# Optimization experiments

Hardware: AMD Instinct MI355X
Metric: run time of the kernel (lower is better)

## Reference

```python
import jax, jax.numpy as jnp
import numpy as np

N_HEAD = 8
LN_EPS = 1e-6


def setup_inputs() -> dict:
    key = jax.random.key(0)
    ks = jax.random.split(key, 6)
    B, S, D = 4, 2048, 256  # D = hidden_size*2 = input_dim
    sc = 1.0 / np.sqrt(D)
    return {
        "inputs": jax.random.normal(ks[0], (B, S, D), jnp.float32),
        "Wq": jax.random.normal(ks[1], (D, D), jnp.float32) * sc,
        "Wk": jax.random.normal(ks[2], (D, D), jnp.float32) * sc,
        "Wv": jax.random.normal(ks[3], (D, D), jnp.float32) * sc,
        "Wf": jax.random.normal(ks[4], (D, D), jnp.float32) * sc,
        "bf": jnp.zeros((D,), jnp.float32),
        "gamma": jnp.ones((D,), jnp.float32),
        "beta": jnp.zeros((D,), jnp.float32),
    }


def reference(inputs, Wq, Wk, Wv, Wf, bf, gamma, beta):
    B, S, D = inputs.shape
    H = N_HEAD
    dh = D // H
    # Projections (torch Linear: x @ W.T), no bias for Q/K/V
    Q = (inputs @ Wq.T).reshape(B, S, H, dh)
    K = (inputs @ Wk.T).reshape(B, S, H, dh)
    V = (inputs @ Wv.T).reshape(B, S, H, dh)
    # NOTE: original scales by sqrt(K.shape[1]) == sqrt(seq_len), not sqrt(dh)
    scale = 1.0 / jnp.sqrt(jnp.float32(S)).astype(inputs.dtype)
    scores = jnp.einsum("bqhd,bkhd->bhqk", Q, K) * scale  # [B,H,S,S]
    attn = jax.nn.softmax(scores, axis=-1)
    out = jnp.einsum("bhqk,bkhd->bqhd", attn, V).reshape(B, S, D)
    out = out @ Wf.T + bf
    # residual + LayerNorm(eps=1e-6)
    x = inputs + out
    mu = jnp.mean(x, axis=-1, keepdims=True)
    var = jnp.mean(jnp.square(x - mu), axis=-1, keepdims=True)
    return (x - mu) * jax.lax.rsqrt(var + LN_EPS) * gamma + beta
```

## Files before the change

kernel.cpp:

```cpp
#include <hip/hip_runtime.h>
#include <hip/hip_bf16.h>

typedef __attribute__((ext_vector_type(8))) short short8;
typedef __attribute__((ext_vector_type(4))) float f32x4;
typedef __attribute__((ext_vector_type(16))) float f32x16;

#define DEVI __device__ __forceinline__

DEVI unsigned short f2bf(float f) {
  union { float f; unsigned int u; } v; v.f = f;
  unsigned int r = v.u + 0x7fffu + ((v.u >> 16) & 1u);
  return (unsigned short)(r >> 16);
}

DEVI unsigned int cvt2(float lo, float hi) {
  unsigned int r;
  asm("v_cvt_pk_bf16_f32 %0, %1, %2" : "=v"(r) : "v"(lo), "v"(hi));
  return r;
}

#define GLDS16(gp, lp)                                                         \
  __builtin_amdgcn_global_load_lds(                                            \
      (const __attribute__((address_space(1))) unsigned int*)(uintptr_t)(gp),  \
      (__attribute__((address_space(3))) unsigned int*)(uintptr_t)(lp), 16, 0, 0)

#define SB 4
#define SS 2048
#define SD 256
#define SH 8
#define SDH 32
#define SM 8192

#define QSCALE 0.0318793654f

#define Q_OFF   0
#define K_OFF   (SM * SD)
#define VT_OFF  (2 * SM * SD)
#define AO_OFF  (3 * SM * SD)

__global__ __launch_bounds__(256) void qkv_k(
    const float* __restrict__ X, const float* __restrict__ Wq,
    const float* __restrict__ Wk, const float* __restrict__ Wv,
    unsigned short* __restrict__ ws) {
  __shared__ __align__(16) unsigned short Atile[128][72];
  __shared__ __align__(16) unsigned short Btile[128][72];
  int tid = threadIdx.x, w = tid >> 6, lane = tid & 63, g = lane >> 4, r = lane & 15;
  int m0 = blockIdx.x * 128, n0 = blockIdx.y * 128;
  int z = n0 >> 8, nbase = n0 & 255;
  const float* Wz = (z == 0) ? Wq : (z == 1) ? Wk : Wv;
  int wr = (w >> 1) * 64, wc = (w & 1) * 64;
  f32x4 acc[4][4] = {};
  int srow = tid >> 3, scol = (tid & 7) * 8;
  float4 a0[4], a1[4], b0[4], b1[4];
#pragma unroll
  for (int p = 0; p < 4; ++p) {
    const float* xa = X + (m0 + srow + p * 32) * SD + scol;
    const float* xb = Wz + (nbase + srow + p * 32) * SD + scol;
    a0[p] = *reinterpret_cast<const float4*>(xa);
    a1[p] = *reinterpret_cast<const float4*>(xa + 4);
    b0[p] = *reinterpret_cast<const float4*>(xb);
    b1[p] = *reinterpret_cast<const float4*>(xb + 4);
  }
  for (int k0 = 0; k0 < SD; k0 += 64) {
    __syncthreads();
#pragma unroll
    for (int p = 0; p < 4; ++p) {
      uint4 ua = { cvt2(a0[p].x, a0[p].y), cvt2(a0[p].z, a0[p].w),
                   cvt2(a1[p].x, a1[p].y), cvt2(a1[p].z, a1[p].w) };
      uint4 ub = { cvt2(b0[p].x, b0[p].y), cvt2(b0[p].z, b0[p].w),
                   cvt2(b1[p].x, b1[p].y), cvt2(b1[p].z, b1[p].w) };
      *reinterpret_cast<uint4*>(&Atile[srow + p * 32][scol]) = ua;
      *reinterpret_cast<uint4*>(&Btile[srow + p * 32][scol]) = ub;
    }
    __syncthreads();
    if (k0 + 64 < SD) {
#pragma unroll
      for (int p = 0; p < 4; ++p) {
        const float* xa = X + (m0 + srow + p * 32) * SD + k0 + 64 + scol;
        const float* xb = Wz + (nbase + srow + p * 32) * SD + k0 + 64 + scol;
        a0[p] = *reinterpret_cast<const float4*>(xa);
        a1[p] = *reinterpret_cast<const float4*>(xa + 4);
        b0[p] = *reinterpret_cast<const float4*>(xb);
        b1[p] = *reinterpret_cast<const float4*>(xb + 4);
      }
    }
#pragma unroll
    for (int ks = 0; ks < 2; ++ks) {
      short8 af[4], bf[4];
#pragma unroll
      for (int i = 0; i < 4; ++i)
        af[i] = *reinterpret_cast<const short8*>(&Atile[wr + i * 16 + r][ks * 32 + g * 8]);
#pragma unroll
      for (int j = 0; j < 4; ++j)
        bf[j] = *reinterpret_cast<const short8*>(&Btile[wc + j * 16 + r][ks * 32 + g * 8]);
#pragma unroll
      for (int i = 0; i < 4; ++i)
#pragma unroll
        for (int j = 0; j < 4; ++j)
          acc[i][j] = __builtin_amdgcn_mfma_f32_16x16x32_bf16(af[i], bf[j], acc[i][j], 0, 0, 0);
    }
  }
  int b_ = m0 >> 11, sbase = m0 & 2047;
  float qs = (z == 0) ? QSCALE : 1.0f;
  unsigned short* Vt = &Btile[0][0];
#pragma unroll
  for (int p = 0; p < 2; ++p) {
    __syncthreads();
    if ((w & 1) == p) {
      if (z < 2) {
#pragma unroll
        for (int i = 0; i < 4; ++i)
#pragma unroll
          for (int j = 0; j < 4; ++j)
#pragma unroll
            for (int jj = 0; jj < 4; ++jj)
              Atile[wr + i * 16 + g * 4 + jj][j * 16 + r] = f2bf(acc[i][j][jj] * qs);
      } else {
#pragma unroll
        for (int i = 0; i < 4; ++i)
#pragma unroll
          for (int j = 0; j < 4; ++j) {
            unsigned short o4[4];
#pragma unroll
            for (int jj = 0; jj < 4; ++jj) o4[jj] = f2bf(acc[i][j][jj]);
            *reinterpret_cast<uint2*>(&Vt[(j * 16 + r) * 136 + wr + i * 16 + g * 4]) =
                *reinterpret_cast<const uint2*>(o4);
          }
      }
    }
    __syncthreads();
    if (z < 2) {
      unsigned short* out = ws + (z == 0 ? Q_OFF : K_OFF);
      int h0 = (nbase + p * 64) >> 5;
#pragma unroll
      for (int it = 0; it < 4; ++it) {
        int c = it * 256 + tid;
        int m = c >> 3, cr = c & 7, hl = cr >> 2, ch = cr & 3;
        short8 val = *reinterpret_cast<const short8*>(&Atile[m][hl * 32 + ch * 8]);
        int h = h0 + hl;
        *reinterpret_cast<short8*>(
            out + (((b_ << 3) + h) * SS + sbase + m) * SDH + ch * 8) = val;
      }
    } else {
      unsigned short* out = ws + VT_OFF;
      int nb = nbase + p * 64;
#pragma unroll
      for (int it = 0; it < 4; ++it) {
        int c = it * 256 + tid;
        int nl = c >> 4, ch = c & 15;
        short8 val = *reinterpret_cast<const short8*>(&Vt[nl * 136 + ch * 8]);
        int col = nb + nl, h = col >> 5, d = col & 31;
        *reinterpret_cast<short8*>(
            out + ((((b_ << 3) + h) << 5) + d) * SS + sbase + ch * 8) = val;
      }
    }
  }
}

__global__ __launch_bounds__(512, 4) void attn_k(const unsigned short* __restrict__ ws_c,
                                                 unsigned short* __restrict__ ws) {
  __shared__ __align__(16) unsigned char smem[65536];
  int tid = threadIdx.x, w = tid >> 6, lane = tid & 63;
  int wg = w >> 2, wl = w & 3, gtid = tid & 255;
  int n32 = lane & 31, hi = lane >> 5;
  int wgid = ((blockIdx.x & 7) << 6) + (blockIdx.x >> 3);
  int bh = wgid >> 4, qb = wgid & 15;
  int q0 = qb * 128 + wl * 32;
  const unsigned short* Qh = ws_c + Q_OFF + bh * (SS * SDH);
  const unsigned short* Kg = ws_c + K_OFF + (bh * SS + wg * 1024) * SDH;
  const unsigned short* Vg = ws_c + VT_OFF + bh * (SDH * SS) + wg * 1024;
  short8 qB0 = *reinterpret_cast<const short8*>(Qh + (q0 + n32) * SDH + 8 * hi);
  short8 qB1 = *reinterpret_cast<const short8*>(Qh + (q0 + n32) * SDH + 16 + 8 * hi);
  unsigned short* Kbuf0 = (unsigned short*)(smem + wg * 16384);
  unsigned short* Kbuf1 = (unsigned short*)(smem + wg * 16384 + 8192);
  unsigned short* Vbuf0 = (unsigned short*)(smem + 32768 + wg * 16384);
  unsigned short* Vbuf1 = (unsigned short*)(smem + 32768 + wg * 16384 + 8192);
  int wv = gtid >> 6;
  int kr = gtid >> 2;
  int kcg = (gtid & 3) ^ ((kr >> 1) & 3);
  const unsigned short* gK0 = Kg + kr * SDH + kcg * 8;
  const unsigned short* gK1 = gK0 + 64 * SDH;
  int vr = gtid >> 4;
  int vcg = (gtid & 15) ^ (vr & 7);
  const unsigned short* gV0 = Vg + vr * SS + vcg * 8;
  const unsigned short* gV1 = gV0 + 16 * SS;
  auto issue = [&](int buf, int tt) {
    char* kd = (char*)(buf ? Kbuf1 : Kbuf0) + wv * 1024;
    char* vd = (char*)(buf ? Vbuf1 : Vbuf0) + wv * 1024;
    GLDS16(gK0 + tt * 4096, kd);
    GLDS16(gK1 + tt * 4096, kd + 4096);
    GLDS16(gV0 + tt * 128, vd);
    GLDS16(gV1 + tt * 128, vd + 4096);
  };
  issue(0, 0);
  f32x16 O = {}, Lf = {};
  union { unsigned int u[4]; short8 sv; } ONES;
  ONES.u[0] = 0x3F803F80u; ONES.u[1] = 0x3F803F80u;
  ONES.u[2] = 0x3F803F80u; ONES.u[3] = 0x3F803F80u;
  int rb = (n32 >> 1) & 3;
  int koff0 = (hi ^ rb) * 8;
  int koff1 = ((2 + hi) ^ rb) * 8;
  int vb7 = n32 & 7;
  for (int t = 0; t < 8; ++t) {
    const unsigned short* Kt = (t & 1) ? Kbuf1 : Kbuf0;
    const unsigned short* Vt = (t & 1) ? Vbuf1 : Vbuf0;
    if (t < 7) {
      issue((t + 1) & 1, t + 1);
      asm volatile("s_waitcnt vmcnt(4)" ::: "memory");
    } else {
      asm volatile("s_waitcnt vmcnt(0)" ::: "memory");
    }
    __builtin_amdgcn_s_barrier();
#pragma unroll
    for (int si = 0; si < 4; ++si) {
      int s = (si + wl) & 3;
      const unsigned short* krow = Kt + (s * 32 + n32) * 32;
      short8 ka = *reinterpret_cast<const short8*>(krow + koff0);
      short8 kb = *reinterpret_cast<const short8*>(krow + koff1);
      f32x16 aC = {};
      __builtin_amdgcn_s_setprio(1);
      aC = __builtin_amdgcn_mfma_f32_32x32x16_bf16(ka, qB0, aC, 0, 0, 0);
      aC = __builtin_amdgcn_mfma_f32_32x32x16_bf16(kb, qB1, aC, 0, 0, 0);
      __builtin_amdgcn_s_setprio(0);
#pragma unroll
      for (int i = 0; i < 16; ++i) aC[i] = __builtin_amdgcn_exp2f(aC[i]);
      unsigned int pk[8];
#pragma unroll
      for (int i = 0; i < 8; ++i) pk[i] = cvt2(aC[2 * i], aC[2 * i + 1]);
      asm("v_permlane32_swap_b32 %0, %1" : "+v"(pk[0]), "+v"(pk[2]));
      asm("v_permlane32_swap_b32 %0, %1" : "+v"(pk[1]), "+v"(pk[3]));
      asm("v_permlane32_swap_b32 %0, %1" : "+v"(pk[4]), "+v"(pk[6]));
      asm("v_permlane32_swap_b32 %0, %1" : "+v"(pk[5]), "+v"(pk[7]));
      union { unsigned int u[4]; short8 sv; } A1, A2;
      A1.u[0] = pk[0]; A1.u[1] = pk[1]; A1.u[2] = pk[2]; A1.u[3] = pk[3];
      A2.u[0] = pk[4]; A2.u[1] = pk[5]; A2.u[2] = pk[6]; A2.u[3] = pk[7];
      const unsigned short* vrow = Vt + n32 * 128;
      short8 vB0 = *reinterpret_cast<const short8*>(vrow + ((s * 4 + hi) ^ vb7) * 8);
      short8 vB1 = *reinterpret_cast<const short8*>(vrow + ((s * 4 + 2 + hi) ^ vb7) * 8);
      __builtin_amdgcn_s_setprio(1);
      O  = __builtin_amdgcn_mfma_f32_32x32x16_bf16(A1.sv, vB0, O, 0, 0, 0);
      O  = __builtin_amdgcn_mfma_f32_32x32x16_bf16(A2.sv, vB1, O, 0, 0, 0);
      Lf = __builtin_amdgcn_mfma_f32_32x32x16_bf16(A1.sv, ONES.sv, Lf, 0, 0, 0);
      Lf = __builtin_amdgcn_mfma_f32_32x32x16_bf16(A2.sv, ONES.sv, Lf, 0, 0, 0);
      __builtin_amdgcn_s_setprio(0);
    }
    __builtin_amdgcn_s_barrier();
  }
  __syncthreads();
  float* OCf = reinterpret_cast<float*>(smem);
  float* LCf = OCf + 16 * 257;
  int p = wl * 64 + lane;
  if (wg == 1) {
#pragma unroll
    for (int i = 0; i < 16; ++i) { OCf[i * 257 + p] = O[i]; LCf[i * 257 + p] = Lf[i]; }
  }
  __syncthreads();
  if (wg == 0) {
    int b = bh >> 3, h = bh & 7;
    unsigned short* AO = ws + AO_OFF;
#pragma unroll
    for (int rr = 0; rr < 16; ++rr) {
      float Ot = O[rr] + OCf[rr * 257 + p];
      float Lt = Lf[rr] + LCf[rr * 257 + p];
      int q = (rr & 3) + 8 * (rr >> 2) + 4 * hi;
      AO[(b * SS + q0 + q) * SD + h * SDH + n32] = f2bf(Ot / Lt);
    }
  }
}

__global__ __launch_bounds__(256) void final_k(
    const unsigned short* __restrict__ ws_c, const float* __restrict__ X,
    const float* __restrict__ Wf, const float* __restrict__ bfv,
    const float* __restrict__ gamma, const float* __restrict__ beta,
    float* __restrict__ out) {
  __shared__ __align__(16) unsigned short Al[32][72];
  __shared__ __align__(16) unsigned short Bl[256][72];
  __shared__ float Cl[32][257];
  const unsigned short* AO = ws_c + AO_OFF;
  int tid = threadIdx.x, w = tid >> 6, lane = tid & 63, g = lane >> 4, r = lane & 15;
  int m0 = blockIdx.x * 32;
  f32x4 acc[2][4] = {};
  int arow = tid >> 3, acol = (tid & 7) * 8;
  for (int k0 = 0; k0 < SD; k0 += 64) {
    short8 av = *reinterpret_cast<const short8*>(AO + (m0 + arow) * SD + k0 + acol);
    float4 w0[8], w1[8];
#pragma unroll
    for (int i = 0; i < 8; i++) {
      const float* wp = Wf + (i * 32 + arow) * SD + k0 + acol;
      w0[i] = *reinterpret_cast<const float4*>(wp);
      w1[i] = *reinterpret_cast<const float4*>(wp + 4);
    }
    __syncthreads();
    *reinterpret_cast<short8*>(&Al[arow][acol]) = av;
#pragma unroll
    for (int i = 0; i < 8; i++) {
      uint4 ub = { cvt2(w0[i].x, w0[i].y), cvt2(w0[i].z, w0[i].w),
                   cvt2(w1[i].x, w1[i].y), cvt2(w1[i].z, w1[i].w) };
      *reinterpret_cast<uint4*>(&Bl[i * 32 + arow][acol]) = ub;
    }
    __syncthreads();
#pragma unroll
    for (int ks = 0; ks < 2; ks++) {
      short8 af0 = *reinterpret_cast<const short8*>(&Al[r][ks * 32 + g * 8]);
      short8 af1 = *reinterpret_cast<const short8*>(&Al[16 + r][ks * 32 + g * 8]);
#pragma unroll
      for (int nt = 0; nt < 4; nt++) {
        short8 bb = *reinterpret_cast<const short8*>(&Bl[w * 64 + nt * 16 + r][ks * 32 + g * 8]);
        acc[0][nt] = __builtin_amdgcn_mfma_f32_16x16x32_bf16(af0, bb, acc[0][nt], 0, 0, 0);
        acc[1][nt] = __builtin_amdgcn_mfma_f32_16x16x32_bf16(af1, bb, acc[1][nt], 0, 0, 0);
      }
    }
  }
#pragma unroll
  for (int rt = 0; rt < 2; rt++)
#pragma unroll
    for (int nt = 0; nt < 4; nt++)
#pragma unroll
      for (int j = 0; j < 4; j++)
        Cl[rt * 16 + g * 4 + j][w * 64 + nt * 16 + r] = acc[rt][nt][j];
  __syncthreads();
  int row = tid >> 3, sub = tid & 7;
  int m = m0 + row;
  float x[32];
  float sum = 0.f, sumsq = 0.f;
#pragma unroll
  for (int i = 0; i < 8; i++) {
    int col = sub * 32 + i * 4;
    float4 xv = *reinterpret_cast<const float4*>(X + m * SD + col);
    float4 bb = *reinterpret_cast<const float4*>(bfv + col);
    x[i * 4 + 0] = Cl[row][col + 0] + xv.x + bb.x;
    x[i * 4 + 1] = Cl[row][col + 1] + xv.y + bb.y;
    x[i * 4 + 2] = Cl[row][col + 2] + xv.z + bb.z;
    x[i * 4 + 3] = Cl[row][col + 3] + xv.w + bb.w;
  }
#pragma unroll
  for (int c = 0; c < 32; c++) { sum += x[c]; sumsq += x[c] * x[c]; }
  sum += __shfl_xor(sum, 1);  sumsq += __shfl_xor(sumsq, 1);
  sum += __shfl_xor(sum, 2);  sumsq += __shfl_xor(sumsq, 2);
  sum += __shfl_xor(sum, 4);  sumsq += __shfl_xor(sumsq, 4);
  float mean = sum * (1.0f / 256.0f);
  float var = sumsq * (1.0f / 256.0f) - mean * mean;
  float rstd = rsqrtf(var + 1e-6f);
#pragma unroll
  for (int i = 0; i < 8; i++) {
    int col = sub * 32 + i * 4;
    float4 gv = *reinterpret_cast<const float4*>(gamma + col);
    float4 bv2 = *reinterpret_cast<const float4*>(beta + col);
    float4 ov;
    ov.x = (x[i * 4 + 0] - mean) * rstd * gv.x + bv2.x;
    ov.y = (x[i * 4 + 1] - mean) * rstd * gv.y + bv2.y;
    ov.z = (x[i * 4 + 2] - mean) * rstd * gv.z + bv2.z;
    ov.w = (x[i * 4 + 3] - mean) * rstd * gv.w + bv2.w;
    *reinterpret_cast<float4*>(out + m * SD + col) = ov;
  }
}

extern "C" void kernel_launch(void* const* d_in, const int* in_sizes, int n_in,
                              void* d_out, int out_size, void* d_ws, size_t ws_size,
                              hipStream_t stream) {
  const float* X  = (const float*)d_in[0];
  const float* Wq = (const float*)d_in[1];
  const float* Wk = (const float*)d_in[2];
  const float* Wv = (const float*)d_in[3];
  const float* Wf = (const float*)d_in[4];
  const float* bf = (const float*)d_in[5];
  const float* gm = (const float*)d_in[6];
  const float* bt = (const float*)d_in[7];
  float* out = (float*)d_out;
  unsigned short* ws = (unsigned short*)d_ws;

  qkv_k<<<dim3(64, 6), 256, 0, stream>>>(X, Wq, Wk, Wv, ws);
  attn_k<<<dim3(512), 512, 0, stream>>>(ws, ws);
  final_k<<<256, 256, 0, stream>>>(ws, X, Wf, bf, gm, bt, out);
}
```

Before: 58.94 us.

## Halve GEMM row tiles and pre-convert Wf to bf16 in projection kernel

The QKV projection kernel now uses 64-row tiles, doubling its grid to 768 blocks, and the output kernel uses 16-row tiles over 512 blocks. This puts more workgroups on the GPU's compute units. Wf is converted to bf16 once inside the projection kernel by the V-projection blocks and stored in workspace, so the final kernel loads bf16 weights directly instead of reloading and converting fp32 Wf in every block. In exchange, each block reuses loaded weight tiles less, and the workspace grows by one extra weight region.

```diff
diff --git a/kernel.cpp b/kernel.cpp
--- a/kernel.cpp
+++ b/kernel.cpp
@@ -37,64 +37,78 @@
 #define K_OFF   (SM * SD)
 #define VT_OFF  (2 * SM * SD)
 #define AO_OFF  (3 * SM * SD)
+#define WF_OFF  (4 * SM * SD)
 
 __global__ __launch_bounds__(256) void qkv_k(
     const float* __restrict__ X, const float* __restrict__ Wq,
     const float* __restrict__ Wk, const float* __restrict__ Wv,
-    unsigned short* __restrict__ ws) {
-  __shared__ __align__(16) unsigned short Atile[128][72];
+    const float* __restrict__ Wf, unsigned short* __restrict__ ws) {
+  __shared__ __align__(16) unsigned short Atile[64][72];
   __shared__ __align__(16) unsigned short Btile[128][72];
   int tid = threadIdx.x, w = tid >> 6, lane = tid & 63, g = lane >> 4, r = lane & 15;
-  int m0 = blockIdx.x * 128, n0 = blockIdx.y * 128;
-  int z = n0 >> 8, nbase = n0 & 255;
+  int m0 = blockIdx.x * 64;
+  int z = blockIdx.y >> 1, nbase = (blockIdx.y & 1) * 128;
   const float* Wz = (z == 0) ? Wq : (z == 1) ? Wk : Wv;
-  int wr = (w >> 1) * 64, wc = (w & 1) * 64;
-  f32x4 acc[4][4] = {};
+  if (z == 2) {
+    int slice = blockIdx.x + (nbase ? 128 : 0);
+    ws[WF_OFF + slice * 256 + tid] = f2bf(Wf[slice * 256 + tid]);
+  }
+  int wr = (w >> 1) * 32, wc = (w & 1) * 64;
+  f32x4 acc[2][4] = {};
   int srow = tid >> 3, scol = (tid & 7) * 8;
-  float4 a0[4], a1[4], b0[4], b1[4];
-#pragma unroll
-  for (int p = 0; p < 4; ++p) {
+  float4 a0[2], a1[2], b0[4], b1[4];
+#pragma unroll
+  for (int p = 0; p < 2; ++p) {
     const float* xa = X + (m0 + srow + p * 32) * SD + scol;
-    const float* xb = Wz + (nbase + srow + p * 32) * SD + scol;
     a0[p] = *reinterpret_cast<const float4*>(xa);
     a1[p] = *reinterpret_cast<const float4*>(xa + 4);
+  }
+#pragma unroll
+  for (int p = 0; p < 4; ++p) {
+    const float* xb = Wz + (nbase + srow + p * 32) * SD + scol;
     b0[p] = *reinterpret_cast<const float4*>(xb);
     b1[p] = *reinterpret_cast<const float4*>(xb + 4);
   }
   for (int k0 = 0; k0 < SD; k0 += 64) {
     __syncthreads();
 #pragma unroll
-    for (int p = 0; p < 4; ++p) {
+    for (int p = 0; p < 2; ++p) {
       uint4 ua = { cvt2(a0[p].x, a0[p].y), cvt2(a0[p].z, a0[p].w),
                    cvt2(a1[p].x, a1[p].y), cvt2(a1[p].z, a1[p].w) };
+      *reinterpret_cast<uint4*>(&Atile[srow + p * 32][scol]) = ua;
+    }
+#pragma unroll
+    for (int p = 0; p < 4; ++p) {
       uint4 ub = { cvt2(b0[p].x, b0[p].y), cvt2(b0[p].z, b0[p].w),
                    cvt2(b1[p].x, b1[p].y), cvt2(b1[p].z, b1[p].w) };
-      *reinterpret_cast<uint4*>(&Atile[srow + p * 32][scol]) = ua;
       *reinterpret_cast<uint4*>(&Btile[srow + p * 32][scol]) = ub;
     }
     __syncthreads();
     if (k0 + 64 < SD) {
 #pragma unroll
-      for (int p = 0; p < 4; ++p) {
+      for (int p = 0; p < 2; ++p) {
         const float* xa = X + (m0 + srow + p * 32) * SD + k0 + 64 + scol;
-        const float* xb = Wz + (nbase + srow + p * 32) * SD + k0 + 64 + scol;
         a0[p] = *reinterpret_cast<const float4*>(xa);
         a1[p] = *reinterpret_cast<const float4*>(xa + 4);
+      }
+#pragma unroll
+      for (int p = 0; p < 4; ++p) {
+        const float* xb = Wz + (nbase + srow + p * 32) * SD + k0 + 64 + scol;
         b0[p] = *reinterpret_cast<const float4*>(xb);
         b1[p] = *reinterpret_cast<const float4*>(xb + 4);
       }
     }
 #pragma unroll
     for (int ks = 0; ks < 2; ++ks) {
-      short8 af[4], bf[4];
-#pragma unroll
-      for (int i = 0; i < 4; ++i)
+      short8 af[2], bf[4];
+#pragma unroll
+      for (int i = 0; i < 2; ++i)
         af[i] = *reinterpret_cast<const short8*>(&Atile[wr + i * 16 + r][ks * 32 + g * 8]);
 #pragma unroll
       for (int j = 0; j < 4; ++j)
         bf[j] = *reinterpret_cast<const short8*>(&Btile[wc + j * 16 + r][ks * 32 + g * 8]);
 #pragma unroll
-      for (int i = 0; i < 4; ++i)
+      for (int i = 0; i < 2; ++i)
 #pragma unroll
         for (int j = 0; j < 4; ++j)
           acc[i][j] = __builtin_amdgcn_mfma_f32_16x16x32_bf16(af[i], bf[j], acc[i][j], 0, 0, 0);
@@ -109,7 +123,7 @@
     if ((w & 1) == p) {
       if (z < 2) {
 #pragma unroll
-        for (int i = 0; i < 4; ++i)
+        for (int i = 0; i < 2; ++i)
 #pragma unroll
           for (int j = 0; j < 4; ++j)
 #pragma unroll
@@ -117,13 +131,13 @@
               Atile[wr + i * 16 + g * 4 + jj][j * 16 + r] = f2bf(acc[i][j][jj] * qs);
       } else {
 #pragma unroll
-        for (int i = 0; i < 4; ++i)
+        for (int i = 0; i < 2; ++i)
 #pragma unroll
           for (int j = 0; j < 4; ++j) {
             unsigned short o4[4];
 #pragma unroll
             for (int jj = 0; jj < 4; ++jj) o4[jj] = f2bf(acc[i][j][jj]);
-            *reinterpret_cast<uint2*>(&Vt[(j * 16 + r) * 136 + wr + i * 16 + g * 4]) =
+            *reinterpret_cast<uint2*>(&Vt[(j * 16 + r) * 80 + wr + i * 16 + g * 4]) =
                 *reinterpret_cast<const uint2*>(o4);
           }
       }
@@ -133,7 +147,7 @@
       unsigned short* out = ws + (z == 0 ? Q_OFF : K_OFF);
       int h0 = (nbase + p * 64) >> 5;
 #pragma unroll
-      for (int it = 0; it < 4; ++it) {
+      for (int it = 0; it < 2; ++it) {
         int c = it * 256 + tid;
         int m = c >> 3, cr = c & 7, hl = cr >> 2, ch = cr & 3;
         short8 val = *reinterpret_cast<const short8*>(&Atile[m][hl * 32 + ch * 8]);
@@ -145,10 +159,10 @@
       unsigned short* out = ws + VT_OFF;
       int nb = nbase + p * 64;
 #pragma unroll
-      for (int it = 0; it < 4; ++it) {
+      for (int it = 0; it < 2; ++it) {
         int c = it * 256 + tid;
-        int nl = c >> 4, ch = c & 15;
-        short8 val = *reinterpret_cast<const short8*>(&Vt[nl * 136 + ch * 8]);
+        int nl = c >> 3, ch = c & 7;
+        short8 val = *reinterpret_cast<const short8*>(&Vt[nl * 80 + ch * 8]);
         int col = nb + nl, h = col >> 5, d = col & 31;
         *reinterpret_cast<short8*>(
             out + ((((b_ << 3) + h) << 5) + d) * SS + sbase + ch * 8) = val;
@@ -270,62 +284,53 @@
 
 __global__ __launch_bounds__(256) void final_k(
     const unsigned short* __restrict__ ws_c, const float* __restrict__ X,
-    const float* __restrict__ Wf, const float* __restrict__ bfv,
-    const float* __restrict__ gamma, const float* __restrict__ beta,
-    float* __restrict__ out) {
-  __shared__ __align__(16) unsigned short Al[32][72];
+    const float* __restrict__ bfv, const float* __restrict__ gamma,
+    const float* __restrict__ beta, float* __restrict__ out) {
+  __shared__ __align__(16) unsigned short Al[16][72];
   __shared__ __align__(16) unsigned short Bl[256][72];
-  __shared__ float Cl[32][257];
+  __shared__ float Cl[16][257];
   const unsigned short* AO = ws_c + AO_OFF;
+  const unsigned short* Wfb = ws_c + WF_OFF;
   int tid = threadIdx.x, w = tid >> 6, lane = tid & 63, g = lane >> 4, r = lane & 15;
-  int m0 = blockIdx.x * 32;
-  f32x4 acc[2][4] = {};
-  int arow = tid >> 3, acol = (tid & 7) * 8;
+  int m0 = blockIdx.x * 16;
+  f32x4 acc[4] = {};
+  int arow = tid >> 4, acol = (tid & 15) * 4;
+  int brow = tid >> 3, bcol = (tid & 7) * 8;
   for (int k0 = 0; k0 < SD; k0 += 64) {
-    short8 av = *reinterpret_cast<const short8*>(AO + (m0 + arow) * SD + k0 + acol);
-    float4 w0[8], w1[8];
-#pragma unroll
-    for (int i = 0; i < 8; i++) {
-      const float* wp = Wf + (i * 32 + arow) * SD + k0 + acol;
-      w0[i] = *reinterpret_cast<const float4*>(wp);
-      w1[i] = *reinterpret_cast<const float4*>(wp + 4);
-    }
-    __syncthreads();
-    *reinterpret_cast<short8*>(&Al[arow][acol]) = av;
-#pragma unroll
-    for (int i = 0; i < 8; i++) {
-      uint4 ub = { cvt2(w0[i].x, w0[i].y), cvt2(w0[i].z, w0[i].w),
-                   cvt2(w1[i].x, w1[i].y), cvt2(w1[i].z, w1[i].w) };
-      *reinterpret_cast<uint4*>(&Bl[i * 32 + arow][acol]) = ub;
-    }
+    uint2 av = *reinterpret_cast<const uint2*>(AO + (m0 + arow) * SD + k0 + acol);
+    short8 bv[8];
+#pragma unroll
+    for (int i = 0; i < 8; i++)
+      bv[i] = *reinterpret_cast<const short8*>(Wfb + (i * 32 + brow) * SD + k0 + bcol);
+    __syncthreads();
+    *reinterpret_cast<uint2*>(&Al[arow][acol]) = av;
+#pragma unroll
+    for (int i = 0; i < 8; i++)
+      *reinterpret_cast<short8*>(&Bl[i * 32 + brow][bcol]) = bv[i];
     __syncthreads();
 #pragma unroll
     for (int ks = 0; ks < 2; ks++) {
-      short8 af0 = *reinterpret_cast<const short8*>(&Al[r][ks * 32 + g * 8]);
-      short8 af1 = *reinterpret_cast<const short8*>(&Al[16 + r][ks * 32 + g * 8]);
+      short8 af = *reinterpret_cast<const short8*>(&Al[r][ks * 32 + g * 8]);
 #pragma unroll
       for (int nt = 0; nt < 4; nt++) {
         short8 bb = *reinterpret_cast<const short8*>(&Bl[w * 64 + nt * 16 + r][ks * 32 + g * 8]);
-        acc[0][nt] = __builtin_amdgcn_mfma_f32_16x16x32_bf16(af0, bb, acc[0][nt], 0, 0, 0);
-        acc[1][nt] = __builtin_amdgcn_mfma_f32_16x16x32_bf16(af1, bb, acc[1][nt], 0, 0, 0);
-      }
-    }
-  }
-#pragma unroll
-  for (int rt = 0; rt < 2; rt++)
-#pragma unroll
-    for (int nt = 0; nt < 4; nt++)
-#pragma unroll
-      for (int j = 0; j < 4; j++)
-        Cl[rt * 16 + g * 4 + j][w * 64 + nt * 16 + r] = acc[rt][nt][j];
+        acc[nt] = __builtin_amdgcn_mfma_f32_16x16x32_bf16(af, bb, acc[nt], 0, 0, 0);
+      }
+    }
+  }
+#pragma unroll
+  for (int nt = 0; nt < 4; nt++)
+#pragma unroll
+    for (int j = 0; j < 4; j++)
+      Cl[g * 4 + j][w * 64 + nt * 16 + r] = acc[nt][j];
   __syncthreads();
-  int row = tid >> 3, sub = tid & 7;
+  int row = tid >> 4, sub = tid & 15;
   int m = m0 + row;
-  float x[32];
+  float x[16];
   float sum = 0.f, sumsq = 0.f;
 #pragma unroll
-  for (int i = 0; i < 8; i++) {
-    int col = sub * 32 + i * 4;
+  for (int i = 0; i < 4; i++) {
+    int col = sub * 16 + i * 4;
     float4 xv = *reinterpret_cast<const float4*>(X + m * SD + col);
     float4 bb = *reinterpret_cast<const float4*>(bfv + col);
     x[i * 4 + 0] = Cl[row][col + 0] + xv.x + bb.x;
@@ -334,16 +339,17 @@
     x[i * 4 + 3] = Cl[row][col + 3] + xv.w + bb.w;
   }
 #pragma unroll
-  for (int c = 0; c < 32; c++) { sum += x[c]; sumsq += x[c] * x[c]; }
+  for (int c = 0; c < 16; c++) { sum += x[c]; sumsq += x[c] * x[c]; }
   sum += __shfl_xor(sum, 1);  sumsq += __shfl_xor(sumsq, 1);
   sum += __shfl_xor(sum, 2);  sumsq += __shfl_xor(sumsq, 2);
   sum += __shfl_xor(sum, 4);  sumsq += __shfl_xor(sumsq, 4);
+  sum += __shfl_xor(sum, 8);  sumsq += __shfl_xor(sumsq, 8);
   float mean = sum * (1.0f / 256.0f);
   float var = sumsq * (1.0f / 256.0f) - mean * mean;
   float rstd = rsqrtf(var + 1e-6f);
 #pragma unroll
-  for (int i = 0; i < 8; i++) {
-    int col = sub * 32 + i * 4;
+  for (int i = 0; i < 4; i++) {
+    int col = sub * 16 + i * 4;
     float4 gv = *reinterpret_cast<const float4*>(gamma + col);
     float4 bv2 = *reinterpret_cast<const float4*>(beta + col);
     float4 ov;
@@ -369,7 +375,7 @@
   float* out = (float*)d_out;
   unsigned short* ws = (unsigned short*)d_ws;
 
-  qkv_k<<<dim3(64, 6), 256, 0, stream>>>(X, Wq, Wk, Wv, ws);
+  qkv_k<<<dim3(128, 6), 256, 0, stream>>>(X, Wq, Wk, Wv, Wf, ws);
   attn_k<<<dim3(512), 512, 0, stream>>>(ws, ws);
-  final_k<<<256, 256, 0, stream>>>(ws, X, Wf, bf, gm, bt, out);
-}
+  final_k<<<512, 256, 0, stream>>>(ws, X, bf, gm, bt, out);
+}
```

Result: faster. 54.77 us, median of 2 (-7.1%).
